# Performance work log

Hardware: AMD Instinct MI355X
Metric: run time of the kernel (lower is better)

## Reference

```python
import jax, jax.numpy as jnp
import numpy as np


def conv1x1(x, w, b):
    # x: [B,C,H,W], w: [O,C], b: [O] -> [B,O,H,W]
    return jnp.einsum('oc,bchw->bohw', w, x) + b[None, :, None, None]


def setup_inputs() -> dict:
    key = jax.random.key(0)
    ks = jax.random.split(key, 9)
    B, C, H, W = 4, 256, 64, 64
    Ci = C // 2
    s_in = 1.0 / np.sqrt(C)
    s_mid = 1.0 / np.sqrt(Ci)
    return {
        'x': jax.random.normal(ks[0], (B, C, H, W), jnp.float32),
        'theta_w': jax.random.normal(ks[1], (Ci, C), jnp.float32) * s_in,
        'theta_b': jnp.zeros((Ci,), jnp.float32),
        'phi_w': jax.random.normal(ks[2], (Ci, C), jnp.float32) * s_in,
        'phi_b': jnp.zeros((Ci,), jnp.float32),
        'g_w': jax.random.normal(ks[3], (Ci, C), jnp.float32) * s_in,
        'g_b': jnp.zeros((Ci,), jnp.float32),
        'out_w': jax.random.normal(ks[4], (C, Ci), jnp.float32) * s_mid,
        'out_b': jnp.zeros((C,), jnp.float32),
    }


def reference(x, theta_w, theta_b, phi_w, phi_b, g_w, g_b, out_w, out_b):
    B, C, H, W = x.shape
    N = H * W
    theta = conv1x1(x, theta_w, theta_b).reshape(B, -1, N)  # [B,Ci,N]
    phi = conv1x1(x, phi_w, phi_b).reshape(B, -1, N)        # [B,Ci,N]
    g = conv1x1(x, g_w, g_b).reshape(B, -1, N)              # [B,Ci,N]
    # attention[b,n,m] = theta[b,:,n] . phi[b,:,m]
    attn = jnp.einsum('bcn,bcm->bnm', theta, phi)           # [B,N,N]
    attn = jax.nn.softmax(attn, axis=-1)
    # out[b,c,n] = sum_m g[b,c,m] * attn[b,n,m]  (g @ attn^T)
    out = jnp.einsum('bcm,bnm->bcn', g, attn).reshape(B, -1, H, W)
    out = conv1x1(out, out_w, out_b)
    return out + x
```

## Files before the change

### kernel.cpp

```cpp
#include <hip/hip_runtime.h>
#include <stdint.h>

#define NB 4
#define NC 256
#define NCI 128
#define NN 4096

typedef __attribute__((ext_vector_type(8))) short short8;
typedef __attribute__((ext_vector_type(4))) float f32x4;

__device__ __forceinline__ float bf2f(unsigned short u) {
    union { unsigned int i; float f; } v; v.i = ((unsigned int)u) << 16; return v.f;
}
__device__ __forceinline__ unsigned short f2bf(float f) {
    union { unsigned int i; float f; } v; v.f = f;
    unsigned int b = v.i;
    b += 0x7FFFu + ((b >> 16) & 1u);
    return (unsigned short)(b >> 16);
}

__global__ void k_fill(float* __restrict__ p, float v, int n) {
    int i = blockIdx.x * blockDim.x + threadIdx.x;
    if (i < n) p[i] = v;
}

__global__ __launch_bounds__(256) void k_split(
    const float* __restrict__ Wt, const float* __restrict__ Wp,
    const float* __restrict__ Wg, const float* __restrict__ Wo,
    unsigned short* __restrict__ wbuf) {
    const float LOG2E = 1.4426950408889634f;
    int m = blockIdx.y;
    int i = blockIdx.x * 256 + threadIdx.x;
    if (m == 0) {
        float v = Wt[i] * LOG2E;
        unsigned short h = f2bf(v);
        wbuf[i] = h;
        wbuf[32768 + i] = f2bf(v - bf2f(h));
    } else if (m == 1) {
        float v = Wp[i];
        unsigned short h = f2bf(v);
        wbuf[65536 + i] = h;
        wbuf[98304 + i] = f2bf(v - bf2f(h));
    } else if (m == 2) {
        wbuf[131072 + i] = f2bf(Wg[i]);
    } else {
        wbuf[163840 + i] = f2bf(Wo[i]);
    }
}

__global__ __launch_bounds__(256, 2) void k_qkv2(
    const float* __restrict__ x,
    const unsigned short* __restrict__ WpH, const unsigned short* __restrict__ WpL,
    const unsigned short* __restrict__ WgH,
    const float* __restrict__ bp, const float* __restrict__ bg,
    unsigned short* __restrict__ phiH, unsigned short* __restrict__ phiL,
    unsigned short* __restrict__ gout) {
    __shared__ __align__(16) unsigned short sXh[32 * 72];
    __shared__ __align__(16) unsigned short sXl[32 * 72];
    const int b = blockIdx.y, n0 = blockIdx.x * 32;
    const int tid = threadIdx.x, lane = tid & 63, wave = tid >> 6;
    const int col = lane & 15, quad = lane >> 4;
    const int wm = wave * 32;

    f32x4 accP[2][2], accG[2][2];
#pragma unroll
    for (int i = 0; i < 2; i++)
#pragma unroll
        for (int j = 0; j < 2; j++)
#pragma unroll
            for (int e = 0; e < 4; e++) { accP[i][j][e] = 0.f; accG[i][j][e] = 0.f; }

    for (int c0 = 0; c0 < NC; c0 += 64) {
        __syncthreads();
        short8 ah[2][2], al[2][2], ag[2][2];
#pragma unroll
        for (int ks = 0; ks < 2; ks++)
#pragma unroll
            for (int i = 0; i < 2; i++) {
                size_t w = (size_t)(wm + i * 16 + col) * NC + c0 + ks * 32 + quad * 8;
                ah[ks][i] = *(const short8*)&WpH[w];
                al[ks][i] = *(const short8*)&WpL[w];
                ag[ks][i] = *(const short8*)&WgH[w];
            }
        {
            int cp = tid >> 3, n4 = (tid & 7) * 4;
            const float* xp = x + ((size_t)(b * NC + c0 + 2 * cp)) * NN + n0 + n4;
            float4 a = *(const float4*)xp;
            float4 c = *(const float4*)(xp + NN);
            float av[4] = { a.x, a.y, a.z, a.w };
            float cv[4] = { c.x, c.y, c.z, c.w };
#pragma unroll
            for (int j = 0; j < 4; j++) {
                unsigned short ha = f2bf(av[j]), hc = f2bf(cv[j]);
                unsigned short la = f2bf(av[j] - bf2f(ha)), lc = f2bf(cv[j] - bf2f(hc));
                *(unsigned int*)&sXh[(n4 + j) * 72 + 2 * cp] =
                    (unsigned int)ha | ((unsigned int)hc << 16);
                *(unsigned int*)&sXl[(n4 + j) * 72 + 2 * cp] =
                    (unsigned int)la | ((unsigned int)lc << 16);
            }
        }
        __syncthreads();
#pragma unroll
        for (int ks = 0; ks < 2; ks++)
#pragma unroll
            for (int j = 0; j < 2; j++) {
                short8 bh = *(const short8*)&sXh[(j * 16 + col) * 72 + ks * 32 + quad * 8];
                short8 bl = *(const short8*)&sXl[(j * 16 + col) * 72 + ks * 32 + quad * 8];
#pragma unroll
                for (int i = 0; i < 2; i++) {
                    accP[i][j] = __builtin_amdgcn_mfma_f32_16x16x32_bf16(ah[ks][i], bh, accP[i][j], 0, 0, 0);
                    accP[i][j] = __builtin_amdgcn_mfma_f32_16x16x32_bf16(ah[ks][i], bl, accP[i][j], 0, 0, 0);
                    accP[i][j] = __builtin_amdgcn_mfma_f32_16x16x32_bf16(al[ks][i], bh, accP[i][j], 0, 0, 0);
                    accG[i][j] = __builtin_amdgcn_mfma_f32_16x16x32_bf16(ag[ks][i], bh, accG[i][j], 0, 0, 0);
                }
            }
    }
#pragma unroll
    for (int i = 0; i < 2; i++) {
        int mrow = wm + i * 16 + quad * 4;
#pragma unroll
        for (int j = 0; j < 2; j++) {
            int n = n0 + j * 16 + col;
            unsigned short h[4], l[4];
#pragma unroll
            for (int e = 0; e < 4; e++) {
                float v = accP[i][j][e] + bp[mrow + e];
                h[e] = f2bf(v);
                l[e] = f2bf(v - bf2f(h[e]));
            }
            uint2 hv, lv;
            hv.x = (unsigned int)h[0] | ((unsigned int)h[1] << 16);
            hv.y = (unsigned int)h[2] | ((unsigned int)h[3] << 16);
            lv.x = (unsigned int)l[0] | ((unsigned int)l[1] << 16);
            lv.y = (unsigned int)l[2] | ((unsigned int)l[3] << 16);
            *(uint2*)&phiH[((size_t)(b * NN + n)) * NCI + mrow] = hv;
            *(uint2*)&phiL[((size_t)(b * NN + n)) * NCI + mrow] = lv;
#pragma unroll
            for (int r = 0; r < 4; r++)
                gout[((size_t)(b * NCI + mrow + r)) * NN + n] = f2bf(accG[i][j][r] + bg[mrow + r]);
        }
    }
}

__global__ __launch_bounds__(1024, 4) void k_attn(
    const float* __restrict__ x,
    const unsigned short* __restrict__ WtH, const unsigned short* __restrict__ WtL,
    const float* __restrict__ bt,
    const unsigned short* __restrict__ phiH, const unsigned short* __restrict__ phiL,
    const unsigned short* __restrict__ gmat,
    const unsigned short* __restrict__ WoH, const float* __restrict__ bo,
    float* __restrict__ y) {
    const float LOG2E = 1.4426950408889634f;
    __shared__ __align__(16) char smem[148480];
    unsigned short* sPhiH0 = (unsigned short*)(smem);
    unsigned short* sPhiH1 = (unsigned short*)(smem + 16384);
    unsigned short* sPhiL0 = (unsigned short*)(smem + 32768);
    unsigned short* sPhiL1 = (unsigned short*)(smem + 49152);
    unsigned short* sGbase = (unsigned short*)(smem + 65536);
    unsigned short* sPall0 = (unsigned short*)(smem + 131072);
    unsigned short* sPall1 = (unsigned short*)(smem + 139264);
    float* sLi             = (float*)(smem + 147456);
    unsigned short* sThH  = (unsigned short*)(smem);
    unsigned short* sThL  = (unsigned short*)(smem + 16384);
    unsigned short* sXhA  = (unsigned short*)(smem + 32768);
    unsigned short* sXlA  = (unsigned short*)(smem + 41984);
    unsigned short* sXhB  = (unsigned short*)(smem + 51200);
    unsigned short* sXlB  = (unsigned short*)(smem + 60416);
    float* sThF           = (float*)(smem + 32768);
    unsigned short* sO    = (unsigned short*)(smem);

    const int id = blockIdx.x;
    const int xcd = id & 7, slot = id >> 3;
    const int b = xcd >> 1;
    const int n0 = (slot * 2 + (xcd & 1)) * 64;

    const int tid = threadIdx.x, lane = tid & 63, wave = tid >> 6;
    const int col = lane & 15, quad = lane >> 4;
    const int qg = wave >> 2, kh = wave & 3;

    uint4 rPh, rPl, rG;
    auto LOADT = [&](int m0) {
        int row = tid >> 4, seg = tid & 15;
        size_t src = ((size_t)(b * NN + m0 + row)) * NCI + seg * 8;
        rPh = *(const uint4*)&phiH[src];
        rPl = *(const uint4*)&phiL[src];
        int row2 = tid >> 3, seg2 = tid & 7;
        rG = *(const uint4*)&gmat[((size_t)(b * NCI + row2)) * NN + m0 + seg2 * 8];
    };
    auto STORET = [&](unsigned short* dPh, unsigned short* dPl, unsigned short* dG) {
        int row = tid >> 4, seg = tid & 15;
        int dst = row * 128 + ((seg * 8) ^ ((row & 7) << 3));
        *(uint4*)&dPh[dst] = rPh;
        *(uint4*)&dPl[dst] = rPl;
        int row2 = tid >> 3, seg2 = tid & 7;
        *(uint4*)&dG[row2 * 64 + ((seg2 * 8) ^ ((row2 & 7) << 3))] = rG;
    };

    const int half = wave >> 3;
    const int wci8 = (wave & 7) * 16;
    f32x4 th[4];
#pragma unroll
    for (int j = 0; j < 4; j++)
#pragma unroll
        for (int e = 0; e < 4; e++) th[j][e] = 0.f;

    for (int s = 0; s < 2; s++) {
        {
            int set = tid >> 9;
            int t = tid & 511;
            int cp = t >> 4, n4 = (t & 15) * 4;
            int myc0 = set * 128 + s * 64;
            unsigned short* dXh = set ? sXhB : sXhA;
            unsigned short* dXl = set ? sXlB : sXlA;
            const float* xp = x + ((size_t)(b * NC + myc0 + 2 * cp)) * NN + n0 + n4;
            float4 a = *(const float4*)xp;
            float4 c = *(const float4*)(xp + NN);
            float av[4] = { a.x, a.y, a.z, a.w };
            float cv[4] = { c.x, c.y, c.z, c.w };
#pragma unroll
            for (int j = 0; j < 4; j++) {
                unsigned short ha = f2bf(av[j]), hc = f2bf(cv[j]);
                unsigned short la = f2bf(av[j] - bf2f(ha)), lc = f2bf(cv[j] - bf2f(hc));
                *(unsigned int*)&dXh[(n4 + j) * 72 + 2 * cp] =
                    (unsigned int)ha | ((unsigned int)hc << 16);
                *(unsigned int*)&dXl[(n4 + j) * 72 + 2 * cp] =
                    (unsigned int)la | ((unsigned int)lc << 16);
            }
        }
        __syncthreads();
        {
            int c0 = half * 128 + s * 64;
            const unsigned short* mXh = half ? sXhB : sXhA;
            const unsigned short* mXl = half ? sXlB : sXlA;
#pragma unroll
            for (int ks = 0; ks < 2; ks++) {
                size_t w = (size_t)(wci8 + col) * NC + c0 + ks * 32 + quad * 8;
                short8 ah = *(const short8*)&WtH[w];
                short8 al = *(const short8*)&WtL[w];
#pragma unroll
                for (int j = 0; j < 4; j++) {
                    short8 bh = *(const short8*)&mXh[(j * 16 + col) * 72 + ks * 32 + quad * 8];
                    short8 bl = *(const short8*)&mXl[(j * 16 + col) * 72 + ks * 32 + quad * 8];
                    th[j] = __builtin_amdgcn_mfma_f32_16x16x32_bf16(ah, bh, th[j], 0, 0, 0);
                    th[j] = __builtin_amdgcn_mfma_f32_16x16x32_bf16(ah, bl, th[j], 0, 0, 0);
                    th[j] = __builtin_amdgcn_mfma_f32_16x16x32_bf16(al, bh, th[j], 0, 0, 0);
                }
            }
        }
        __syncthreads();
    }
    if (half == 0) {
#pragma unroll
        for (int j = 0; j < 4; j++) {
            int q = j * 16 + col;
            int ci = (wci8 + quad * 4) ^ ((q & 7) << 2);
            *(f32x4*)&sThF[q * 128 + ci] = th[j];
        }
    }
    __syncthreads();
    if (half == 1) {
#pragma unroll
        for (int j = 0; j < 4; j++) {
            int q = j * 16 + col;
            int cif = (wci8 + quad * 4) ^ ((q & 7) << 2);
            f32x4 o = *(const f32x4*)&sThF[q * 128 + cif];
            unsigned short h[4], l[4];
#pragma unroll
            for (int e = 0; e < 4; e++) {
                float v = o[e] + th[j][e] + bt[wci8 + quad * 4 + e] * LOG2E;
                h[e] = f2bf(v);
                l[e] = f2bf(v - bf2f(h[e]));
            }
            int cisw = (wci8 + quad * 4) ^ ((q & 7) << 3);
            uint2 hv, lv;
            hv.x = (unsigned int)h[0] | ((unsigned int)h[1] << 16);
            hv.y = (unsigned int)h[2] | ((unsigned int)h[3] << 16);
            lv.x = (unsigned int)l[0] | ((unsigned int)l[1] << 16);
            lv.y = (unsigned int)l[2] | ((unsigned int)l[3] << 16);
            *(uint2*)&sThH[q * 128 + cisw] = hv;
            *(uint2*)&sThL[q * 128 + cisw] = lv;
        }
    }
    __syncthreads();
    short8 qh[4], ql[4];
    {
        int qrow = qg * 16 + col;
        int qsw = (qrow & 7) << 3;
#pragma unroll
        for (int ks = 0; ks < 4; ks++) {
            int off = (ks * 32 + quad * 8) ^ qsw;
            qh[ks] = *(const short8*)&sThH[qrow * 128 + off];
            ql[ks] = *(const short8*)&sThL[qrow * 128 + off];
        }
    }
    LOADT(0);
    __syncthreads();
    STORET(sPhiH0, sPhiL0, sGbase);
    LOADT(64);
    __syncthreads();

    f32x4 oacc[2];
#pragma unroll
    for (int i = 0; i < 2; i++)
#pragma unroll
        for (int e = 0; e < 4; e++) oacc[i][e] = 0.f;
    float li[4] = { 0.f, 0.f, 0.f, 0.f };

    auto step = [&](const unsigned short* cPhiH, const unsigned short* cPhiL,
                    unsigned short* nPhiH, unsigned short* nPhiL,
                    unsigned short* wG, const unsigned short* rGb,
                    unsigned short* wPall, const unsigned short* rPall,
                    int m_next, bool do_pv) {
        STORET(nPhiH, nPhiL, wG);
        LOADT(m_next);

        f32x4 S;
#pragma unroll
        for (int e = 0; e < 4; e++) S[e] = 0.f;
        {
            int kcol = kh * 16 + col;
            int kswz = (kcol & 7) << 3;
#pragma unroll
            for (int ks = 0; ks < 4; ks++) {
                int off = (ks * 32 + quad * 8) ^ kswz;
                short8 ph = *(const short8*)&cPhiH[kcol * 128 + off];
                short8 pl = *(const short8*)&cPhiL[kcol * 128 + off];
                S = __builtin_amdgcn_mfma_f32_16x16x32_bf16(qh[ks], ph, S, 0, 0, 0);
                S = __builtin_amdgcn_mfma_f32_16x16x32_bf16(qh[ks], pl, S, 0, 0, 0);
                S = __builtin_amdgcn_mfma_f32_16x16x32_bf16(ql[ks], ph, S, 0, 0, 0);
            }
        }
        if (do_pv) {
            short8 pf[2], af[2][2];
            int qrow = qg * 16 + col;
            int qsw = (qrow & 7) << 3;
#pragma unroll
            for (int ks = 0; ks < 2; ks++)
                pf[ks] = *(const short8*)&rPall[qrow * 64 + ((ks * 32 + quad * 8) ^ qsw)];
#pragma unroll
            for (int ct = 0; ct < 2; ct++) {
                int grow = kh * 32 + ct * 16 + col;
                int gsw = (grow & 7) << 3;
#pragma unroll
                for (int ks = 0; ks < 2; ks++)
                    af[ct][ks] = *(const short8*)&rGb[grow * 64 + ((ks * 32 + quad * 8) ^ gsw)];
            }
#pragma unroll
            for (int ct = 0; ct < 2; ct++)
#pragma unroll
                for (int ks = 0; ks < 2; ks++)
                    oacc[ct] = __builtin_amdgcn_mfma_f32_16x16x32_bf16(
                        af[ct][ks], pf[ks], oacc[ct], 0, 0, 0);
        }
#pragma unroll
        for (int r = 0; r < 4; r++) {
            float p = exp2f(S[r]);
            li[r] += p;
            int q = qg * 16 + quad * 4 + r;
            wPall[q * 64 + ((kh * 16 + col) ^ ((q & 7) << 3))] = f2bf(p);
        }
        __syncthreads();
    };

    int gwA = 8192, grA = 24576, gwB = 16384, grB = 0;
    for (int it = 0; it < 32; ++it) {
        int mA = it * 128 + 128; if (mA > 4032) mA = 4032;
        int mB = it * 128 + 192; if (mB > 4032) mB = 4032;
        step(sPhiH0, sPhiL0, sPhiH1, sPhiL1, sGbase + gwA, sGbase + grA,
             sPall0, sPall1, mA, it != 0);
        step(sPhiH1, sPhiL1, sPhiH0, sPhiL0, sGbase + gwB, sGbase + grB,
             sPall1, sPall0, mB, true);
        gwA ^= 16384; grA ^= 16384; gwB ^= 16384; grB ^= 16384;
    }
    {
        short8 pf[2], af[2][2];
        int qrow = qg * 16 + col;
        int qsw = (qrow & 7) << 3;
#pragma unroll
        for (int ks = 0; ks < 2; ks++)
            pf[ks] = *(const short8*)&sPall1[qrow * 64 + ((ks * 32 + quad * 8) ^ qsw)];
#pragma unroll
        for (int ct = 0; ct < 2; ct++) {
            int grow = kh * 32 + ct * 16 + col;
            int gsw = (grow & 7) << 3;
#pragma unroll
            for (int ks = 0; ks < 2; ks++)
                af[ct][ks] = *(const short8*)&sGbase[24576 + grow * 64 + ((ks * 32 + quad * 8) ^ gsw)];
        }
#pragma unroll
        for (int ct = 0; ct < 2; ct++)
#pragma unroll
            for (int ks = 0; ks < 2; ks++)
                oacc[ct] = __builtin_amdgcn_mfma_f32_16x16x32_bf16(
                    af[ct][ks], pf[ks], oacc[ct], 0, 0, 0);
    }

#pragma unroll
    for (int r = 0; r < 4; r++) {
        float rs = li[r];
#pragma unroll
        for (int off = 1; off < 16; off <<= 1) rs += __shfl_xor(rs, off);
        li[r] = rs;
    }
    if (col == 0) {
#pragma unroll
        for (int r = 0; r < 4; r++) sLi[wave * 16 + quad * 4 + r] = li[r];
    }
    __syncthreads();
    float inv = 1.0f / (sLi[(qg * 4 + 0) * 16 + col] + sLi[(qg * 4 + 1) * 16 + col] +
                        sLi[(qg * 4 + 2) * 16 + col] + sLi[(qg * 4 + 3) * 16 + col]);

#pragma unroll
    for (int ct = 0; ct < 2; ct++) {
        int q = qg * 16 + col;
        int ci = kh * 32 + ct * 16 + quad * 4;
        int cisw = ci ^ ((q & 7) << 3);
        uint2 v;
        unsigned short p0 = f2bf(oacc[ct][0] * inv);
        unsigned short p1 = f2bf(oacc[ct][1] * inv);
        unsigned short p2 = f2bf(oacc[ct][2] * inv);
        unsigned short p3 = f2bf(oacc[ct][3] * inv);
        v.x = (unsigned int)p0 | ((unsigned int)p1 << 16);
        v.y = (unsigned int)p2 | ((unsigned int)p3 << 16);
        *(uint2*)&sO[q * 128 + cisw] = v;
    }
    __syncthreads();
    f32x4 acc[4];
#pragma unroll
    for (int j = 0; j < 4; j++)
#pragma unroll
        for (int e = 0; e < 4; e++) acc[j][e] = 0.f;
#pragma unroll
    for (int ks = 0; ks < 4; ks++) {
        short8 af2 = *(const short8*)&WoH[(size_t)(wave * 16 + col) * NCI + ks * 32 + quad * 8];
#pragma unroll
        for (int j = 0; j < 4; j++) {
            int row = j * 16 + col;
            short8 bf = *(const short8*)&sO[row * 128 + ((ks * 32 + quad * 8) ^ ((row & 7) << 3))];
            acc[j] = __builtin_amdgcn_mfma_f32_16x16x32_bf16(af2, bf, acc[j], 0, 0, 0);
        }
    }
#pragma unroll
    for (int j = 0; j < 4; j++)
#pragma unroll
        for (int e = 0; e < 4; e++) {
            int o = wave * 16 + quad * 4 + e;
            size_t idx = ((size_t)(b * NC + o)) * NN + n0 + j * 16 + col;
            y[idx] = acc[j][e] + bo[o] + x[idx];
        }
}

extern "C" void kernel_launch(void* const* d_in, const int* in_sizes, int n_in,
                              void* d_out, int out_size, void* d_ws, size_t ws_size,
                              hipStream_t stream) {
    float* y = (float*)d_out;

    bool sizes_ok = (n_in == 9) &&
        in_sizes[0] == NB * NC * NN && in_sizes[1] == NCI * NC && in_sizes[2] == NCI &&
        in_sizes[3] == NCI * NC && in_sizes[4] == NCI && in_sizes[5] == NCI * NC &&
        in_sizes[6] == NCI && in_sizes[7] == NC * NCI && in_sizes[8] == NC &&
        out_size == NB * NC * NN;
    if (!sizes_ok) {
        k_fill<<<(out_size + 255) / 256, 256, 0, stream>>>(y, 777.0f, out_size);
        return;
    }
    if (ws_size < (size_t)16 * 1024 * 1024) {
        k_fill<<<(out_size + 255) / 256, 256, 0, stream>>>(y, 555.0f, out_size);
        return;
    }

    const float* x  = (const float*)d_in[0];
    const float* tw = (const float*)d_in[1];
    const float* tb = (const float*)d_in[2];
    const float* pw = (const float*)d_in[3];
    const float* pb = (const float*)d_in[4];
    const float* gw = (const float*)d_in[5];
    const float* gb = (const float*)d_in[6];
    const float* ow = (const float*)d_in[7];
    const float* obias = (const float*)d_in[8];

    unsigned short* ws16 = (unsigned short*)d_ws;
    unsigned short* phiH = ws16;
    unsigned short* phiL = ws16 + 2097152;
    unsigned short* g    = ws16 + 4194304;
    unsigned short* wbuf = ws16 + 6291456;
    unsigned short* WtH = wbuf,           *WtL = wbuf + 32768;
    unsigned short* WpH = wbuf + 65536,   *WpL = wbuf + 98304;
    unsigned short* WgH = wbuf + 131072,  *WoH = wbuf + 163840;

    k_split<<<dim3(128, 4), 256, 0, stream>>>(tw, pw, gw, ow, wbuf);
    k_qkv2<<<dim3(128, NB), 256, 0, stream>>>(x, WpH, WpL, WgH, pb, gb, phiH, phiL, g);
    k_attn<<<dim3(256), 1024, 0, stream>>>(x, WtH, WtL, tb, phiH, phiL, g, WoH, obias, y);
}
```

Measured before the change: 189.7 us.

## Fuse weight split, phi/g projection and attention into one cooperative kernel

Merges the three kernel launches into a single cooperative kernel of 256 blocks x 1024 threads. Grid-wide barriers separate the weight bf16 split, the phi/g projection and the attention phase. The projection phase is retiled so each 1024-thread block covers 64 positions with a 128-channel K step. This removes two launch gaps and the tail idle time between kernels. In exchange it adds grid.sync overhead and requires all 256 blocks to be co-resident, and the projection runs at the attention kernel's occupancy.

```diff
diff --git a/kernel.cpp b/kernel.cpp
--- a/kernel.cpp
+++ b/kernel.cpp
@@ -1,4 +1,5 @@
 #include <hip/hip_runtime.h>
+#include <hip/hip_cooperative_groups.h>
 #include <stdint.h>
 
 #define NB 4
@@ -24,134 +25,141 @@
     if (i < n) p[i] = v;
 }
 
-__global__ __launch_bounds__(256) void k_split(
-    const float* __restrict__ Wt, const float* __restrict__ Wp,
-    const float* __restrict__ Wg, const float* __restrict__ Wo,
-    unsigned short* __restrict__ wbuf) {
+__global__ __launch_bounds__(1024, 4) void k_fused(
+    const float* __restrict__ x,
+    const float* __restrict__ tw, const float* __restrict__ tb,
+    const float* __restrict__ pw, const float* __restrict__ pb,
+    const float* __restrict__ gw, const float* __restrict__ gb,
+    const float* __restrict__ ow, const float* __restrict__ obias,
+    unsigned short* __restrict__ ws16, float* __restrict__ y) {
     const float LOG2E = 1.4426950408889634f;
-    int m = blockIdx.y;
-    int i = blockIdx.x * 256 + threadIdx.x;
-    if (m == 0) {
-        float v = Wt[i] * LOG2E;
-        unsigned short h = f2bf(v);
-        wbuf[i] = h;
-        wbuf[32768 + i] = f2bf(v - bf2f(h));
-    } else if (m == 1) {
-        float v = Wp[i];
-        unsigned short h = f2bf(v);
-        wbuf[65536 + i] = h;
-        wbuf[98304 + i] = f2bf(v - bf2f(h));
-    } else if (m == 2) {
-        wbuf[131072 + i] = f2bf(Wg[i]);
-    } else {
-        wbuf[163840 + i] = f2bf(Wo[i]);
-    }
-}
-
-__global__ __launch_bounds__(256, 2) void k_qkv2(
-    const float* __restrict__ x,
-    const unsigned short* __restrict__ WpH, const unsigned short* __restrict__ WpL,
-    const unsigned short* __restrict__ WgH,
-    const float* __restrict__ bp, const float* __restrict__ bg,
-    unsigned short* __restrict__ phiH, unsigned short* __restrict__ phiL,
-    unsigned short* __restrict__ gout) {
-    __shared__ __align__(16) unsigned short sXh[32 * 72];
-    __shared__ __align__(16) unsigned short sXl[32 * 72];
-    const int b = blockIdx.y, n0 = blockIdx.x * 32;
+    namespace cg = cooperative_groups;
+    cg::grid_group grid = cg::this_grid();
+
+    unsigned short* phiH = ws16;
+    unsigned short* phiL = ws16 + 2097152;
+    unsigned short* gmat = ws16 + 4194304;
+    unsigned short* wbuf = ws16 + 6291456;
+    const unsigned short* WtH = wbuf;
+    const unsigned short* WtL = wbuf + 32768;
+    const unsigned short* WpH = wbuf + 65536;
+    const unsigned short* WpL = wbuf + 98304;
+    const unsigned short* WgH = wbuf + 131072;
+    const unsigned short* WoH = wbuf + 163840;
+
+    __shared__ __align__(16) char smem[148480];
+
+    const int id = blockIdx.x;
     const int tid = threadIdx.x, lane = tid & 63, wave = tid >> 6;
     const int col = lane & 15, quad = lane >> 4;
-    const int wm = wave * 32;
-
-    f32x4 accP[2][2], accG[2][2];
-#pragma unroll
-    for (int i = 0; i < 2; i++)
+
+    {
+        int gid = id * 1024 + tid;
+        if (gid < 131072) {
+            int m = gid >> 15, i = gid & 32767;
+            if (m == 0) {
+                float v = tw[i] * LOG2E;
+                unsigned short h = f2bf(v);
+                wbuf[i] = h;
+                wbuf[32768 + i] = f2bf(v - bf2f(h));
+            } else if (m == 1) {
+                float v = pw[i];
+                unsigned short h = f2bf(v);
+                wbuf[65536 + i] = h;
+                wbuf[98304 + i] = f2bf(v - bf2f(h));
+            } else if (m == 2) {
+                wbuf[131072 + i] = f2bf(gw[i]);
+            } else {
+                wbuf[163840 + i] = f2bf(ow[i]);
+            }
+        }
+    }
+    __threadfence();
+    grid.sync();
+
+    {
+        unsigned short* sXh = (unsigned short*)(smem);
+        unsigned short* sXl = (unsigned short*)(smem + 17408);
+        const int b2 = id >> 6, n0b = (id & 63) * 64;
+        const int cig = wave >> 1, nh = wave & 1;
+        const int wm16 = cig * 16;
+
+        f32x4 accP[2], accG[2];
 #pragma unroll
         for (int j = 0; j < 2; j++)
 #pragma unroll
-            for (int e = 0; e < 4; e++) { accP[i][j][e] = 0.f; accG[i][j][e] = 0.f; }
-
-    for (int c0 = 0; c0 < NC; c0 += 64) {
-        __syncthreads();
-        short8 ah[2][2], al[2][2], ag[2][2];
-#pragma unroll
-        for (int ks = 0; ks < 2; ks++)
-#pragma unroll
-            for (int i = 0; i < 2; i++) {
-                size_t w = (size_t)(wm + i * 16 + col) * NC + c0 + ks * 32 + quad * 8;
-                ah[ks][i] = *(const short8*)&WpH[w];
-                al[ks][i] = *(const short8*)&WpL[w];
-                ag[ks][i] = *(const short8*)&WgH[w];
-            }
+            for (int e = 0; e < 4; e++) { accP[j][e] = 0.f; accG[j][e] = 0.f; }
+
+        for (int c0 = 0; c0 < NC; c0 += 128) {
+            if (c0) __syncthreads();
+            {
+                int cp = tid >> 4, n4 = (tid & 15) * 4;
+                const float* xp = x + ((size_t)(b2 * NC + c0 + 2 * cp)) * NN + n0b + n4;
+                float4 a = *(const float4*)xp;
+                float4 c = *(const float4*)(xp + NN);
+                float av[4] = { a.x, a.y, a.z, a.w };
+                float cv[4] = { c.x, c.y, c.z, c.w };
+#pragma unroll
+                for (int j = 0; j < 4; j++) {
+                    unsigned short ha = f2bf(av[j]), hc = f2bf(cv[j]);
+                    unsigned short la = f2bf(av[j] - bf2f(ha)), lc = f2bf(cv[j] - bf2f(hc));
+                    *(unsigned int*)&sXh[(n4 + j) * 136 + 2 * cp] =
+                        (unsigned int)ha | ((unsigned int)hc << 16);
+                    *(unsigned int*)&sXl[(n4 + j) * 136 + 2 * cp] =
+                        (unsigned int)la | ((unsigned int)lc << 16);
+                }
+            }
+            __syncthreads();
+            short8 ah[4], al[4], ag[4];
+#pragma unroll
+            for (int ks = 0; ks < 4; ks++) {
+                size_t w = (size_t)(wm16 + col) * NC + c0 + ks * 32 + quad * 8;
+                ah[ks] = *(const short8*)&WpH[w];
+                al[ks] = *(const short8*)&WpL[w];
+                ag[ks] = *(const short8*)&WgH[w];
+            }
+#pragma unroll
+            for (int ks = 0; ks < 4; ks++)
+#pragma unroll
+                for (int j = 0; j < 2; j++) {
+                    int nrow = nh * 32 + j * 16 + col;
+                    short8 bh = *(const short8*)&sXh[nrow * 136 + ks * 32 + quad * 8];
+                    short8 bl = *(const short8*)&sXl[nrow * 136 + ks * 32 + quad * 8];
+                    accP[j] = __builtin_amdgcn_mfma_f32_16x16x32_bf16(ah[ks], bh, accP[j], 0, 0, 0);
+                    accP[j] = __builtin_amdgcn_mfma_f32_16x16x32_bf16(ah[ks], bl, accP[j], 0, 0, 0);
+                    accP[j] = __builtin_amdgcn_mfma_f32_16x16x32_bf16(al[ks], bh, accP[j], 0, 0, 0);
+                    accG[j] = __builtin_amdgcn_mfma_f32_16x16x32_bf16(ag[ks], bh, accG[j], 0, 0, 0);
+                }
+        }
         {
-            int cp = tid >> 3, n4 = (tid & 7) * 4;
-            const float* xp = x + ((size_t)(b * NC + c0 + 2 * cp)) * NN + n0 + n4;
-            float4 a = *(const float4*)xp;
-            float4 c = *(const float4*)(xp + NN);
-            float av[4] = { a.x, a.y, a.z, a.w };
-            float cv[4] = { c.x, c.y, c.z, c.w };
-#pragma unroll
-            for (int j = 0; j < 4; j++) {
-                unsigned short ha = f2bf(av[j]), hc = f2bf(cv[j]);
-                unsigned short la = f2bf(av[j] - bf2f(ha)), lc = f2bf(cv[j] - bf2f(hc));
-                *(unsigned int*)&sXh[(n4 + j) * 72 + 2 * cp] =
-                    (unsigned int)ha | ((unsigned int)hc << 16);
-                *(unsigned int*)&sXl[(n4 + j) * 72 + 2 * cp] =
-                    (unsigned int)la | ((unsigned int)lc << 16);
-            }
-        }
-        __syncthreads();
-#pragma unroll
-        for (int ks = 0; ks < 2; ks++)
+            int mrow = wm16 + quad * 4;
 #pragma unroll
             for (int j = 0; j < 2; j++) {
-                short8 bh = *(const short8*)&sXh[(j * 16 + col) * 72 + ks * 32 + quad * 8];
-                short8 bl = *(const short8*)&sXl[(j * 16 + col) * 72 + ks * 32 + quad * 8];
-#pragma unroll
-                for (int i = 0; i < 2; i++) {
-                    accP[i][j] = __builtin_amdgcn_mfma_f32_16x16x32_bf16(ah[ks][i], bh, accP[i][j], 0, 0, 0);
-                    accP[i][j] = __builtin_amdgcn_mfma_f32_16x16x32_bf16(ah[ks][i], bl, accP[i][j], 0, 0, 0);
-                    accP[i][j] = __builtin_amdgcn_mfma_f32_16x16x32_bf16(al[ks][i], bh, accP[i][j], 0, 0, 0);
-                    accG[i][j] = __builtin_amdgcn_mfma_f32_16x16x32_bf16(ag[ks][i], bh, accG[i][j], 0, 0, 0);
+                int n = n0b + nh * 32 + j * 16 + col;
+                unsigned short h[4], l[4];
+#pragma unroll
+                for (int e = 0; e < 4; e++) {
+                    float v = accP[j][e] + pb[mrow + e];
+                    h[e] = f2bf(v);
+                    l[e] = f2bf(v - bf2f(h[e]));
                 }
-            }
-    }
-#pragma unroll
-    for (int i = 0; i < 2; i++) {
-        int mrow = wm + i * 16 + quad * 4;
-#pragma unroll
-        for (int j = 0; j < 2; j++) {
-            int n = n0 + j * 16 + col;
-            unsigned short h[4], l[4];
-#pragma unroll
-            for (int e = 0; e < 4; e++) {
-                float v = accP[i][j][e] + bp[mrow + e];
-                h[e] = f2bf(v);
-                l[e] = f2bf(v - bf2f(h[e]));
-            }
-            uint2 hv, lv;
-            hv.x = (unsigned int)h[0] | ((unsigned int)h[1] << 16);
-            hv.y = (unsigned int)h[2] | ((unsigned int)h[3] << 16);
-            lv.x = (unsigned int)l[0] | ((unsigned int)l[1] << 16);
-            lv.y = (unsigned int)l[2] | ((unsigned int)l[3] << 16);
-            *(uint2*)&phiH[((size_t)(b * NN + n)) * NCI + mrow] = hv;
-            *(uint2*)&phiL[((size_t)(b * NN + n)) * NCI + mrow] = lv;
-#pragma unroll
-            for (int r = 0; r < 4; r++)
-                gout[((size_t)(b * NCI + mrow + r)) * NN + n] = f2bf(accG[i][j][r] + bg[mrow + r]);
-        }
-    }
-}
-
-__global__ __launch_bounds__(1024, 4) void k_attn(
-    const float* __restrict__ x,
-    const unsigned short* __restrict__ WtH, const unsigned short* __restrict__ WtL,
-    const float* __restrict__ bt,
-    const unsigned short* __restrict__ phiH, const unsigned short* __restrict__ phiL,
-    const unsigned short* __restrict__ gmat,
-    const unsigned short* __restrict__ WoH, const float* __restrict__ bo,
-    float* __restrict__ y) {
-    const float LOG2E = 1.4426950408889634f;
-    __shared__ __align__(16) char smem[148480];
+                uint2 hv, lv;
+                hv.x = (unsigned int)h[0] | ((unsigned int)h[1] << 16);
+                hv.y = (unsigned int)h[2] | ((unsigned int)h[3] << 16);
+                lv.x = (unsigned int)l[0] | ((unsigned int)l[1] << 16);
+                lv.y = (unsigned int)l[2] | ((unsigned int)l[3] << 16);
+                *(uint2*)&phiH[((size_t)(b2 * NN + n)) * NCI + mrow] = hv;
+                *(uint2*)&phiL[((size_t)(b2 * NN + n)) * NCI + mrow] = lv;
+#pragma unroll
+                for (int r = 0; r < 4; r++)
+                    gmat[((size_t)(b2 * NCI + mrow + r)) * NN + n] =
+                        f2bf(accG[j][r] + gb[mrow + r]);
+            }
+        }
+    }
+    __threadfence();
+    grid.sync();
+
     unsigned short* sPhiH0 = (unsigned short*)(smem);
     unsigned short* sPhiH1 = (unsigned short*)(smem + 16384);
     unsigned short* sPhiL0 = (unsigned short*)(smem + 32768);
@@ -169,13 +177,9 @@
     float* sThF           = (float*)(smem + 32768);
     unsigned short* sO    = (unsigned short*)(smem);
 
-    const int id = blockIdx.x;
     const int xcd = id & 7, slot = id >> 3;
     const int b = xcd >> 1;
     const int n0 = (slot * 2 + (xcd & 1)) * 64;
-
-    const int tid = threadIdx.x, lane = tid & 63, wave = tid >> 6;
-    const int col = lane & 15, quad = lane >> 4;
     const int qg = wave >> 2, kh = wave & 3;
 
     uint4 rPh, rPl, rG;
@@ -204,6 +208,7 @@
 #pragma unroll
         for (int e = 0; e < 4; e++) th[j][e] = 0.f;
 
+    __syncthreads();
     for (int s = 0; s < 2; s++) {
         {
             int set = tid >> 9;
@@ -216,11 +221,11 @@
             float4 a = *(const float4*)xp;
             float4 c = *(const float4*)(xp + NN);
             float av[4] = { a.x, a.y, a.z, a.w };
-            float cv[4] = { c.x, c.y, c.z, c.w };
+            float cv4[4] = { c.x, c.y, c.z, c.w };
 #pragma unroll
             for (int j = 0; j < 4; j++) {
-                unsigned short ha = f2bf(av[j]), hc = f2bf(cv[j]);
-                unsigned short la = f2bf(av[j] - bf2f(ha)), lc = f2bf(cv[j] - bf2f(hc));
+                unsigned short ha = f2bf(av[j]), hc = f2bf(cv4[j]);
+                unsigned short la = f2bf(av[j] - bf2f(ha)), lc = f2bf(cv4[j] - bf2f(hc));
                 *(unsigned int*)&dXh[(n4 + j) * 72 + 2 * cp] =
                     (unsigned int)ha | ((unsigned int)hc << 16);
                 *(unsigned int*)&dXl[(n4 + j) * 72 + 2 * cp] =
@@ -267,7 +272,7 @@
             unsigned short h[4], l[4];
 #pragma unroll
             for (int e = 0; e < 4; e++) {
-                float v = o[e] + th[j][e] + bt[wci8 + quad * 4 + e] * LOG2E;
+                float v = o[e] + th[j][e] + tb[wci8 + quad * 4 + e] * LOG2E;
                 h[e] = f2bf(v);
                 l[e] = f2bf(v - bf2f(h[e]));
             }
@@ -446,7 +451,7 @@
         for (int e = 0; e < 4; e++) {
             int o = wave * 16 + quad * 4 + e;
             size_t idx = ((size_t)(b * NC + o)) * NN + n0 + j * 16 + col;
-            y[idx] = acc[j][e] + bo[o] + x[idx];
+            y[idx] = acc[j][e] + obias[o] + x[idx];
         }
 }
 
@@ -478,17 +483,10 @@
     const float* gb = (const float*)d_in[6];
     const float* ow = (const float*)d_in[7];
     const float* obias = (const float*)d_in[8];
-
     unsigned short* ws16 = (unsigned short*)d_ws;
-    unsigned short* phiH = ws16;
-    unsigned short* phiL = ws16 + 2097152;
-    unsigned short* g    = ws16 + 4194304;
-    unsigned short* wbuf = ws16 + 6291456;
-    unsigned short* WtH = wbuf,           *WtL = wbuf + 32768;
-    unsigned short* WpH = wbuf + 65536,   *WpL = wbuf + 98304;
-    unsigned short* WgH = wbuf + 131072,  *WoH = wbuf + 163840;
-
-    k_split<<<dim3(128, 4), 256, 0, stream>>>(tw, pw, gw, ow, wbuf);
-    k_qkv2<<<dim3(128, NB), 256, 0, stream>>>(x, WpH, WpL, WgH, pb, gb, phiH, phiL, g);
-    k_attn<<<dim3(256), 1024, 0, stream>>>(x, WtH, WtL, tb, phiH, phiL, g, WoH, obias, y);
+
+    void* args[] = { (void*)&x, (void*)&tw, (void*)&tb, (void*)&pw, (void*)&pb,
+                     (void*)&gw, (void*)&gb, (void*)&ow, (void*)&obias,
+                     (void*)&ws16, (void*)&y };
+    hipLaunchCooperativeKernel((void*)k_fused, dim3(256), dim3(1024), args, 0, stream);
 }
```

Measured after the change: 472.5 us. +149.1%, slower.
